# Kernel optimization log

Measured on AMD Instinct MI355X. Metric: run time of the kernel, lower is better.

## Reference

```python
import jax, jax.numpy as jnp
import numpy as np

CHUNK = 1024
HEAD_DIM = 128

def setup_inputs() -> dict:
    key = jax.random.key(0)
    k1, k2, k3 = jax.random.split(key, 3)
    B, H, S, D = 2, 16, 4096, HEAD_DIM
    q = jax.random.normal(k1, (B, H, S, D), dtype=jnp.float32)
    k = jax.random.normal(k2, (B, H, S, D), dtype=jnp.float32)
    v = jax.random.normal(k3, (B, H, S, D), dtype=jnp.float32)
    return {"q": q, "k": k, "v": v}

def reference(q, k, v):
    # Faithful to the torch module INCLUDING its masking bug: for every chunk
    # the triu mask uses diagonal=1 in chunk-local coordinates, so chunk-local
    # query row i attends only keys j<=i, i.e. only the first CHUNK keys matter.
    B, H, S, D = q.shape
    scale = D ** (-0.5)
    n = S // CHUNK
    qc = q.reshape(B, H, n, CHUNK, D)           # [B,H,n,C,D]
    kc = k[:, :, :CHUNK, :]                      # [B,H,C,D]
    vc = v[:, :, :CHUNK, :]                      # [B,H,C,D]
    scores = jnp.einsum('bhnid,bhjd->bhnij', qc, kc) * scale  # [B,H,n,C,C]
    mask = jnp.triu(jnp.ones((CHUNK, CHUNK), dtype=bool), 1)   # j > i masked
    scores = jnp.where(mask, -jnp.inf, scores)
    probs = jax.nn.softmax(scores, axis=-1)
    out = jnp.einsum('bhnij,bhjd->bhnid', probs, vc)
    return out.reshape(B, H, S, D)
```

## Files before the change

kernel.cpp:

```cpp
#include <hip/hip_runtime.h>


typedef __attribute__((ext_vector_type(8))) short bfrag_t;
typedef __attribute__((ext_vector_type(16))) float f32x16;
typedef unsigned short u16;
typedef unsigned int   u32;

#define SEQ     4096
#define SCHUNK  1024
#define HD      128
#define NT2     8
#define TILE_E2 16384

__device__ __forceinline__ u16 f2bf(float f) {
    union { float f; unsigned u; } x; x.f = f;
    unsigned r = x.u + 0x7fffu + ((x.u >> 16) & 1u);
    return (u16)(r >> 16);
}

__global__ __launch_bounds__(256)
void mea_prep(const float* __restrict__ kg, const float* __restrict__ vg,
              u16* __restrict__ wsK, u16* __restrict__ wsV)
{
    const int tid  = threadIdx.x;
    const int tile = blockIdx.x;
    const int bh = tile >> 3, kt = tile & 7;
    const long gsrc = (long)bh * SEQ * HD + (long)kt * 128 * HD;
    const long gdst = (long)tile * TILE_E2;

#pragma unroll
    for (int i = 0; i < 8; ++i) {
        int oid = i * 256 + tid;
        int s = oid >> 7, j = oid & 127;
        const float* kp = kg + gsrc + j * HD + s * 8;
        float4 a = *(const float4*)kp;
        float4 b = *(const float4*)(kp + 4);
        bfrag_t f;
        f[0]=f2bf(a.x); f[1]=f2bf(a.y); f[2]=f2bf(a.z); f[3]=f2bf(a.w);
        f[4]=f2bf(b.x); f[5]=f2bf(b.y); f[6]=f2bf(b.z); f[7]=f2bf(b.w);
        *(bfrag_t*)(wsK + gdst + (s * 128 + j) * 8) = f;
    }
#pragma unroll
    for (int i = 0; i < 8; ++i) {
        int oid = i * 256 + tid;
        int sv = oid >> 7, d = oid & 127;
        const float* vp = vg + gsrc + sv * 8 * HD + d;
        bfrag_t f;
#pragma unroll
        for (int jj = 0; jj < 8; ++jj) f[jj] = f2bf(vp[jj * HD]);
        *(bfrag_t*)(wsV + gdst + (sv * 128 + d) * 8) = f;
    }
}

__device__ __forceinline__ void gll16(const u16* g, u16* l) {
    __builtin_amdgcn_global_load_lds((const __attribute__((address_space(1))) u32*)g,
                                     (__attribute__((address_space(3))) u32*)l, 16, 0, 0);
}

__device__ __forceinline__ float tsum16(const f32x16& p) {
    float a0 = (p[0] + p[1]) + (p[2] + p[3]);
    float a1 = (p[4] + p[5]) + (p[6] + p[7]);
    float a2 = (p[8] + p[9]) + (p[10] + p[11]);
    float a3 = (p[12] + p[13]) + (p[14] + p[15]);
    return (a0 + a1) + (a2 + a3);
}

__device__ __forceinline__ void sm_cvt(f32x16& s, float& lsum, bfrag_t* pf) {
#pragma unroll
    for (int r = 0; r < 16; ++r) s[r] = exp2f(s[r]);
    lsum += tsum16(s);
    u32 W[8];
#pragma unroll
    for (int t2 = 0; t2 < 8; ++t2)
        asm("v_cvt_pk_bf16_f32 %0, %1, %2"
            : "=v"(W[t2]) : "v"(s[2 * t2]), "v"(s[2 * t2 + 1]));
#pragma unroll
    for (int u2 = 0; u2 < 2; ++u2) {
        u32 x0 = W[4 * u2 + 0], y0 = W[4 * u2 + 2];
        u32 x1 = W[4 * u2 + 1], y1 = W[4 * u2 + 3];
        asm("v_permlane32_swap_b32 %0, %1" : "+v"(x0), "+v"(y0));
        asm("v_permlane32_swap_b32 %0, %1" : "+v"(x1), "+v"(y1));
        union { u32 w[4]; bfrag_t f; } cvt;
        cvt.w[0] = x0; cvt.w[1] = x1; cvt.w[2] = y0; cvt.w[3] = y1;
        pf[u2] = cvt.f;
    }
}

__global__ __launch_bounds__(512, 2)
void mea_main(const float* __restrict__ qg, const u16* __restrict__ wsK,
              const u16* __restrict__ wsV, float* __restrict__ og)
{
    __shared__ __align__(16) u16 K_s[2][TILE_E2];
    __shared__ __align__(16) u16 V_s[2][TILE_E2];

    const int tid  = threadIdx.x;
    const int lane = tid & 63;
    const int wv   = tid >> 6;
    const int c31  = lane & 31;
    const int hi   = lane >> 5;
    const int ch   = wv & 3;
    const int h    = wv >> 2;

    const int x   = blockIdx.x & 7;
    const int idx = blockIdx.x >> 3;
    const int bh  = x * 4 + (idx & 3);
    const int p   = idx >> 2;

    const long bhrow = (long)bh * SEQ + (long)ch * SCHUNK + (long)h * 32;
    const u16* Kb = wsK + (long)bh * NT2 * TILE_E2;
    const u16* Vb = wsV + (long)bh * NT2 * TILE_E2;
    const int so   = wv * 2048 + lane * 8;
    const int ldsb = wv * 2048;
    const float qs = 0.12751723f;

    const int kfo = hi * 1024 + c31 * 8;
    const int vfo = hi * 1024 + c31 * 8;

#pragma unroll
    for (int c = 0; c < 4; ++c) {
        gll16(Kb + so + c * 512, &K_s[0][ldsb + c * 512]);
        gll16(Vb + so + c * 512, &V_s[0][ldsb + c * 512]);
    }

    int cur = 0;
    for (int seg = 0; seg < 2; ++seg) {
        const int qt  = seg ? p : (15 - p);
        const int nt2 = (qt >> 1) + 1;
        const long rowbase = bhrow + (long)qt * 64;

        bfrag_t qf[8];
        {
            const float* qp = qg + (rowbase + c31) * HD + hi * 8;
#pragma unroll
            for (int ks = 0; ks < 8; ++ks) {
                float4 a = *(const float4*)(qp + ks * 16);
                float4 b = *(const float4*)(qp + ks * 16 + 4);
                bfrag_t f;
                f[0]=f2bf(a.x*qs); f[1]=f2bf(a.y*qs); f[2]=f2bf(a.z*qs); f[3]=f2bf(a.w*qs);
                f[4]=f2bf(b.x*qs); f[5]=f2bf(b.y*qs); f[6]=f2bf(b.z*qs); f[7]=f2bf(b.w*qs);
                qf[ks] = f;
            }
        }

        f32x16 oacc[4];
#pragma unroll
        for (int d = 0; d < 4; ++d)
#pragma unroll
            for (int i = 0; i < 16; ++i) oacc[d][i] = 0.f;
        float lsum = 0.f;

        for (int kt = 0; kt < nt2; ++kt) {
            __syncthreads();

            if (kt + 1 < nt2) {
                const long tb = (long)(kt + 1) * TILE_E2;
#pragma unroll
                for (int c = 0; c < 4; ++c) {
                    gll16(Kb + tb + so + c * 512, &K_s[cur ^ 1][ldsb + c * 512]);
                    gll16(Vb + tb + so + c * 512, &V_s[cur ^ 1][ldsb + c * 512]);
                }
            } else if (seg == 0) {
#pragma unroll
                for (int c = 0; c < 4; ++c) {
                    gll16(Kb + so + c * 512, &K_s[cur ^ 1][ldsb + c * 512]);
                    gll16(Vb + so + c * 512, &V_s[cur ^ 1][ldsb + c * 512]);
                }
            }

            const bool last  = (kt == nt2 - 1);
            const int  gdiag = last ? ((qt * 64 + h * 32 - kt * 128) >> 5) : 4;

            const u16* kbase = &K_s[cur][kfo];
            const u16* vbase = &V_s[cur][vfo];

#pragma unroll
            for (int g = 0; g < 4; ++g) {
                if (g <= gdiag) {
                    const bool tri = (g == gdiag);
                    f32x16 s;
#pragma unroll
                    for (int i = 0; i < 16; ++i) s[i] = 0.f;
                    __builtin_amdgcn_s_setprio(1);
#pragma unroll
                    for (int ks = 0; ks < 8; ++ks) {
                        bfrag_t kf = *(const bfrag_t*)(kbase + ks * 2048 + g * 256);
                        s = __builtin_amdgcn_mfma_f32_32x32x16_bf16(kf, qf[ks], s, 0, 0, 0);
                    }
                    __builtin_amdgcn_s_setprio(0);
                    if (tri) {
#pragma unroll
                        for (int r = 0; r < 16; ++r) {
                            int crow = (r & 3) + 8 * (r >> 2) + 4 * hi;
                            if (crow > c31) s[r] = -1e30f;
                        }
                    }
                    bfrag_t pf[2];
                    sm_cvt(s, lsum, pf);
                    __builtin_amdgcn_s_setprio(1);
#pragma unroll
                    for (int dg = 0; dg < 4; ++dg) {
#pragma unroll
                        for (int j2 = 0; j2 < 2; ++j2) {
                            bfrag_t vf = *(const bfrag_t*)(vbase + (g * 2 + j2) * 2048 + dg * 256);
                            oacc[dg] = __builtin_amdgcn_mfma_f32_32x32x16_bf16(vf, pf[j2], oacc[dg], 0, 0, 0);
                        }
                    }
                    __builtin_amdgcn_s_setprio(0);
                }
            }

            cur ^= 1;
        }

        lsum += __shfl_xor(lsum, 32);
        float inv = 1.f / lsum;
#pragma unroll
        for (int dg = 0; dg < 4; ++dg) {
#pragma unroll
            for (int rq = 0; rq < 4; ++rq) {
                float4 v;
                v.x = oacc[dg][rq * 4 + 0] * inv;
                v.y = oacc[dg][rq * 4 + 1] * inv;
                v.z = oacc[dg][rq * 4 + 2] * inv;
                v.w = oacc[dg][rq * 4 + 3] * inv;
                *(float4*)(og + (rowbase + c31) * HD + dg * 32 + rq * 8 + hi * 4) = v;
            }
        }
    }
}

extern "C" void kernel_launch(void* const* d_in, const int* in_sizes, int n_in,
                              void* d_out, int out_size, void* d_ws, size_t ws_size,
                              hipStream_t stream)
{
    (void)in_sizes; (void)n_in; (void)out_size; (void)ws_size;
    const float* q = (const float*)d_in[0];
    const float* k = (const float*)d_in[1];
    const float* v = (const float*)d_in[2];
    float* o = (float*)d_out;
    u16* wsK = (u16*)d_ws;
    u16* wsV = wsK + (size_t)32 * NT2 * TILE_E2;
    mea_prep<<<dim3(256), dim3(256), 0, stream>>>(k, v, wsK, wsV);
    mea_main<<<dim3(256), dim3(512), 0, stream>>>(q, wsK, wsV, o);
}
```

Before: 68.48 us.

## Stage only K in LDS with 256-key tiles; load V fragments from global

The prep kernel now packs K into 256-key tiles, and the main kernel double-buffers only K in shared memory while reading V fragments straight from global (L2) memory, prefetched at the start of each 32-key group. This halves the number of barrier-synchronised tile iterations and removes the V LDS staging. LDS use per block stays the same. In exchange, each wave issues its own global loads for V, which raises global/L2 traffic and exposes load latency that LDS double-buffering used to hide.

```diff
diff --git a/kernel.cpp b/kernel.cpp
--- a/kernel.cpp
+++ b/kernel.cpp
@@ -9,8 +9,9 @@
 #define SEQ     4096
 #define SCHUNK  1024
 #define HD      128
-#define NT2     8
-#define TILE_E2 16384
+#define NTK     4
+#define KTILE_E 32768
+#define VTILE_E 16384
 
 __device__ __forceinline__ u16 f2bf(float f) {
     union { float f; unsigned u; } x; x.f = f;
@@ -26,8 +27,8 @@
     const int tile = blockIdx.x;
     const int bh = tile >> 3, kt = tile & 7;
     const long gsrc = (long)bh * SEQ * HD + (long)kt * 128 * HD;
-    const long gdst = (long)tile * TILE_E2;
-
+
+    const long kdst = ((long)bh * 4 + (kt >> 1)) * KTILE_E + (long)(kt & 1) * 128 * 8;
 #pragma unroll
     for (int i = 0; i < 8; ++i) {
         int oid = i * 256 + tid;
@@ -38,8 +39,9 @@
         bfrag_t f;
         f[0]=f2bf(a.x); f[1]=f2bf(a.y); f[2]=f2bf(a.z); f[3]=f2bf(a.w);
         f[4]=f2bf(b.x); f[5]=f2bf(b.y); f[6]=f2bf(b.z); f[7]=f2bf(b.w);
-        *(bfrag_t*)(wsK + gdst + (s * 128 + j) * 8) = f;
-    }
+        *(bfrag_t*)(wsK + kdst + ((long)s * 256 + j) * 8) = f;
+    }
+    const long vdst = (long)tile * VTILE_E;
 #pragma unroll
     for (int i = 0; i < 8; ++i) {
         int oid = i * 256 + tid;
@@ -48,7 +50,7 @@
         bfrag_t f;
 #pragma unroll
         for (int jj = 0; jj < 8; ++jj) f[jj] = f2bf(vp[jj * HD]);
-        *(bfrag_t*)(wsV + gdst + (sv * 128 + d) * 8) = f;
+        *(bfrag_t*)(wsV + vdst + (sv * 128 + d) * 8) = f;
     }
 }
 
@@ -90,8 +92,7 @@
 void mea_main(const float* __restrict__ qg, const u16* __restrict__ wsK,
               const u16* __restrict__ wsV, float* __restrict__ og)
 {
-    __shared__ __align__(16) u16 K_s[2][TILE_E2];
-    __shared__ __align__(16) u16 V_s[2][TILE_E2];
+    __shared__ __align__(16) u16 K_s[2][KTILE_E];
 
     const int tid  = threadIdx.x;
     const int lane = tid & 63;
@@ -107,25 +108,23 @@
     const int p   = idx >> 2;
 
     const long bhrow = (long)bh * SEQ + (long)ch * SCHUNK + (long)h * 32;
-    const u16* Kb = wsK + (long)bh * NT2 * TILE_E2;
-    const u16* Vb = wsV + (long)bh * NT2 * TILE_E2;
-    const int so   = wv * 2048 + lane * 8;
-    const int ldsb = wv * 2048;
+    const u16* Kb = wsK + (long)bh * NTK * KTILE_E;
+    const u16* Vb = wsV + (long)bh * 8 * VTILE_E;
+    const int so   = wv * 4096 + lane * 8;
+    const int ldsb = wv * 4096;
     const float qs = 0.12751723f;
 
-    const int kfo = hi * 1024 + c31 * 8;
+    const int kfo = hi * 2048 + c31 * 8;
     const int vfo = hi * 1024 + c31 * 8;
 
 #pragma unroll
-    for (int c = 0; c < 4; ++c) {
+    for (int c = 0; c < 8; ++c)
         gll16(Kb + so + c * 512, &K_s[0][ldsb + c * 512]);
-        gll16(Vb + so + c * 512, &V_s[0][ldsb + c * 512]);
-    }
 
     int cur = 0;
     for (int seg = 0; seg < 2; ++seg) {
         const int qt  = seg ? p : (15 - p);
-        const int nt2 = (qt >> 1) + 1;
+        const int ntk = (qt >> 2) + 1;
         const long rowbase = bhrow + (long)qt * 64;
 
         bfrag_t qf[8];
@@ -149,45 +148,48 @@
             for (int i = 0; i < 16; ++i) oacc[d][i] = 0.f;
         float lsum = 0.f;
 
-        for (int kt = 0; kt < nt2; ++kt) {
+        for (int kt = 0; kt < ntk; ++kt) {
             __syncthreads();
 
-            if (kt + 1 < nt2) {
-                const long tb = (long)(kt + 1) * TILE_E2;
-#pragma unroll
-                for (int c = 0; c < 4; ++c) {
+            if (kt + 1 < ntk) {
+                const long tb = (long)(kt + 1) * KTILE_E;
+#pragma unroll
+                for (int c = 0; c < 8; ++c)
                     gll16(Kb + tb + so + c * 512, &K_s[cur ^ 1][ldsb + c * 512]);
-                    gll16(Vb + tb + so + c * 512, &V_s[cur ^ 1][ldsb + c * 512]);
-                }
             } else if (seg == 0) {
 #pragma unroll
-                for (int c = 0; c < 4; ++c) {
+                for (int c = 0; c < 8; ++c)
                     gll16(Kb + so + c * 512, &K_s[cur ^ 1][ldsb + c * 512]);
-                    gll16(Vb + so + c * 512, &V_s[cur ^ 1][ldsb + c * 512]);
-                }
-            }
-
-            const bool last  = (kt == nt2 - 1);
-            const int  gdiag = last ? ((qt * 64 + h * 32 - kt * 128) >> 5) : 4;
+            }
+
+            const bool last  = (kt == ntk - 1);
+            const int  gdiag = last ? ((qt * 64 + h * 32 - kt * 256) >> 5) : 8;
 
             const u16* kbase = &K_s[cur][kfo];
-            const u16* vbase = &V_s[cur][vfo];
-
-#pragma unroll
-            for (int g = 0; g < 4; ++g) {
+
+#pragma unroll
+            for (int g = 0; g < 8; ++g) {
                 if (g <= gdiag) {
-                    const bool tri = (g == gdiag);
+                    const int jg = kt * 8 + g;
+                    const u16* vb = Vb + (jg >> 2) * VTILE_E + (jg & 3) * 4096 + vfo;
+                    bfrag_t vf[8];
+#pragma unroll
+                    for (int j2 = 0; j2 < 2; ++j2)
+#pragma unroll
+                        for (int dg = 0; dg < 4; ++dg)
+                            vf[j2 * 4 + dg] = *(const bfrag_t*)(vb + j2 * 2048 + dg * 256);
+
                     f32x16 s;
 #pragma unroll
                     for (int i = 0; i < 16; ++i) s[i] = 0.f;
                     __builtin_amdgcn_s_setprio(1);
 #pragma unroll
                     for (int ks = 0; ks < 8; ++ks) {
-                        bfrag_t kf = *(const bfrag_t*)(kbase + ks * 2048 + g * 256);
+                        bfrag_t kf = *(const bfrag_t*)(kbase + ks * 4096 + g * 256);
                         s = __builtin_amdgcn_mfma_f32_32x32x16_bf16(kf, qf[ks], s, 0, 0, 0);
                     }
                     __builtin_amdgcn_s_setprio(0);
-                    if (tri) {
+                    if (g == gdiag) {
 #pragma unroll
                         for (int r = 0; r < 16; ++r) {
                             int crow = (r & 3) + 8 * (r >> 2) + 4 * hi;
@@ -196,14 +198,12 @@
                     }
                     bfrag_t pf[2];
                     sm_cvt(s, lsum, pf);
+
                     __builtin_amdgcn_s_setprio(1);
 #pragma unroll
                     for (int dg = 0; dg < 4; ++dg) {
-#pragma unroll
-                        for (int j2 = 0; j2 < 2; ++j2) {
-                            bfrag_t vf = *(const bfrag_t*)(vbase + (g * 2 + j2) * 2048 + dg * 256);
-                            oacc[dg] = __builtin_amdgcn_mfma_f32_32x32x16_bf16(vf, pf[j2], oacc[dg], 0, 0, 0);
-                        }
+                        oacc[dg] = __builtin_amdgcn_mfma_f32_32x32x16_bf16(vf[dg],     pf[0], oacc[dg], 0, 0, 0);
+                        oacc[dg] = __builtin_amdgcn_mfma_f32_32x32x16_bf16(vf[4 + dg], pf[1], oacc[dg], 0, 0, 0);
                     }
                     __builtin_amdgcn_s_setprio(0);
                 }
@@ -239,7 +239,7 @@
     const float* v = (const float*)d_in[2];
     float* o = (float*)d_out;
     u16* wsK = (u16*)d_ws;
-    u16* wsV = wsK + (size_t)32 * NT2 * TILE_E2;
+    u16* wsV = wsK + (size_t)32 * NTK * KTILE_E;
     mea_prep<<<dim3(256), dim3(256), 0, stream>>>(k, v, wsK, wsV);
     mea_main<<<dim3(256), dim3(512), 0, stream>>>(q, wsK, wsV, o);
 }
```

Measured after the change: 70.76 us. +3.3%, slower.
